# Optimization experiments

Measured on AMD Instinct MI355X. Metric: run time of the kernel, lower is better.

## Reference

```python
import jax, jax.numpy as jnp
import numpy as np

B, S, DM, H = 16, 4096, 512, 4
HD = DM // H  # head_dim = 128
EPS = 1e-5


def setup_inputs() -> dict:
    key = jax.random.key(0)
    ks = jax.random.split(key, 9)
    sc = 1.0 / np.sqrt(DM)
    inp = {
        "x": jax.random.normal(ks[0], (B, S, DM), dtype=jnp.float32),
        "Wq_w": jax.random.normal(ks[1], (DM, DM), dtype=jnp.float32) * sc,
        "Wq_b": jnp.zeros((DM,), dtype=jnp.float32),
        "Wk_w": jax.random.normal(ks[2], (DM, DM), dtype=jnp.float32) * sc,
        "Wk_b": jnp.zeros((DM,), dtype=jnp.float32),
        "Wv_w": jax.random.normal(ks[3], (DM, DM), dtype=jnp.float32) * sc,
        "Wv_b": jnp.zeros((DM,), dtype=jnp.float32),
        "Wo_w": jax.random.normal(ks[4], (DM, DM), dtype=jnp.float32) * sc,
        "Wo_b": jnp.zeros((DM,), dtype=jnp.float32),
        "ln_g": jnp.ones((DM,), dtype=jnp.float32),
        "ln_b": jnp.zeros((DM,), dtype=jnp.float32),
    }
    return inp


def _forward(x, Wq_w, Wq_b, Wk_w, Wk_b, Wv_w, Wv_b, Wo_w, Wo_b, ln_g, ln_b):
    b, s, _ = x.shape
    # Linear projections, viewed as [B,S,H,HD] exactly as the torch code does
    Q = (x @ Wq_w.T + Wq_b).reshape(b, s, H, HD)
    K = (x @ Wk_w.T + Wk_b).reshape(b, s, H, HD)
    V = (x @ Wv_w.T + Wv_b).reshape(b, s, H, HD)
    # NOTE: source never permutes heads to dim 1, so attention is over the
    # HEAD axis per token: scores [B,S,H,H]
    scores = jnp.einsum("bshd,bstd->bsht", Q, K) / np.sqrt(HD).astype(np.float32)
    attn = jax.nn.softmax(scores, axis=-1)  # dropout is identity in eval
    out = jnp.einsum("bsht,bstd->bshd", attn, V).reshape(b, s, DM)
    out = out @ Wo_w.T + Wo_b
    y = out + x  # input_dim == output_dim -> residual branch taken
    mu = jnp.mean(y, axis=-1, keepdims=True)
    var = jnp.mean((y - mu) ** 2, axis=-1, keepdims=True)
    return (y - mu) * jax.lax.rsqrt(var + EPS) * ln_g + ln_b


def reference(x, Wq_w, Wq_b, Wk_w, Wk_b, Wv_w, Wv_b, Wo_w, Wo_b, ln_g, ln_b):
    return _forward(x, Wq_w, Wq_b, Wk_w, Wk_b, Wv_w, Wv_b, Wo_w, Wo_b, ln_g, ln_b)
```

## Files before the change

kernel.cpp:

```cpp
#include <hip/hip_runtime.h>
#include <stdint.h>

#define NTOK 65536
#define DMODEL 512
#define QKVN 1536
#define LN_EPS 1e-5f

typedef __attribute__((ext_vector_type(8))) short short8;
typedef __attribute__((ext_vector_type(8))) unsigned short ushort8;
typedef __attribute__((ext_vector_type(4))) float float4_t;

static __device__ __forceinline__ float bf2f(unsigned short u) {
    union { unsigned int i; float f; } c; c.i = ((unsigned int)u) << 16; return c.f;
}
static __device__ __forceinline__ unsigned short f2bf(float f) {
    union { float f; unsigned int i; } c; c.f = f;
    unsigned int x = c.i;
    return (unsigned short)((x + 0x7fffu + ((x >> 16) & 1u)) >> 16);
}
static __device__ __forceinline__ void gload_lds16(const void* g, void* l) {
    __builtin_amdgcn_global_load_lds((const __attribute__((address_space(1))) void*)g,
                                     (__attribute__((address_space(3))) void*)l, 16, 0, 0);
}

#define BAR() __builtin_amdgcn_s_barrier()
#define WAITL0() asm volatile("s_waitcnt lgkmcnt(0)" ::: "memory")
#define WVM(n) asm volatile("s_waitcnt vmcnt(" #n ")" ::: "memory")
#define MFMA(a, b, c) __builtin_amdgcn_mfma_f32_16x16x32_bf16((a), (b), (c), 0, 0, 0)

__global__ __launch_bounds__(256) void cast_x_kernel(const float* __restrict__ x,
                                                     unsigned short* __restrict__ xb, int n8) {
    int stride = gridDim.x * blockDim.x;
    for (int i = blockIdx.x * blockDim.x + threadIdx.x; i < n8; i += stride) {
        const float4_t* p = (const float4_t*)(x + (size_t)i * 8);
        float4_t a = p[0], b = p[1];
        ushort8 v;
        v[0] = f2bf(a[0]); v[1] = f2bf(a[1]); v[2] = f2bf(a[2]); v[3] = f2bf(a[3]);
        v[4] = f2bf(b[0]); v[5] = f2bf(b[1]); v[6] = f2bf(b[2]); v[7] = f2bf(b[3]);
        *(ushort8*)(xb + (size_t)i * 8) = v;
    }
}

__global__ __launch_bounds__(256) void prep_w_kernel(
    const float* __restrict__ wq, const float* __restrict__ wk, const float* __restrict__ wv,
    const float* __restrict__ wo,
    const float* __restrict__ bq, const float* __restrict__ bk, const float* __restrict__ bv,
    unsigned short* __restrict__ wqkv, unsigned short* __restrict__ wob,
    float* __restrict__ bias_qkv) {
    const int WN = DMODEL * DMODEL;
    int tid = blockIdx.x * blockDim.x + threadIdx.x;
    int stride = gridDim.x * blockDim.x;
    for (int j = tid; j < 3 * WN; j += stride) {
        int seg = j / WN, idx = j - seg * WN;
        const float* src = (seg == 0) ? wq : (seg == 1) ? wk : wv;
        wqkv[j] = f2bf(src[idx]);
    }
    for (int j = tid; j < WN; j += stride) wob[j] = f2bf(wo[j]);
    for (int j = tid; j < QKVN; j += stride)
        bias_qkv[j] = (j < 512) ? bq[j] : (j < 1024) ? bk[j - 512] : bv[j - 1024];
}

__global__ __launch_bounds__(512, 2) void gemm1_kernel(
    const unsigned short* __restrict__ A, const unsigned short* __restrict__ Bw,
    const float* __restrict__ bias, unsigned short* __restrict__ Cout) {
    __shared__ unsigned short As[4][256 * 32];
    __shared__ unsigned short Bs[4][256 * 32];

    const int b = blockIdx.x;
    const int L = (b & 7) * 192 + (b >> 3);
    const int bm = L / 6;
    const int bn = L - bm * 6;

    const int t = threadIdx.x;
    const int lane = t & 63;
    const int w = t >> 6;
    const int wm = w >> 2, wn = w & 3;

    const unsigned short* Ab = A + (size_t)bm * 256 * 512;
    const unsigned short* Bb = Bw + (size_t)bn * 256 * 512;

    const int i0 = t, i1 = 512 + t;
    const int r0 = i0 >> 2, s0 = (i0 & 3) ^ ((r0 >> 1) & 3);
    const int r1 = i1 >> 2, s1 = (i1 & 3) ^ ((r1 >> 1) & 3);

#define STAGE_A1(kt) do { \
        gload_lds16(Ab + r0 * 512 + (kt) * 32 + s0 * 8, &As[(kt) & 3][i0 * 8]); \
        gload_lds16(Ab + r1 * 512 + (kt) * 32 + s1 * 8, &As[(kt) & 3][i1 * 8]); } while (0)
#define STAGE_B1(kt) do { \
        gload_lds16(Bb + r0 * 512 + (kt) * 32 + s0 * 8, &Bs[(kt) & 3][i0 * 8]); \
        gload_lds16(Bb + r1 * 512 + (kt) * 32 + s1 * 8, &Bs[(kt) & 3][i1 * 8]); } while (0)

    int aoff[8], boff[4];
#pragma unroll
    for (int m = 0; m < 8; m++) {
        int row = wm * 128 + m * 16 + (lane & 15);
        aoff[m] = row * 32 + (((lane >> 4) ^ ((row >> 1) & 3)) * 8);
    }
#pragma unroll
    for (int n = 0; n < 4; n++) {
        int row = wn * 64 + n * 16 + (lane & 15);
        boff[n] = row * 32 + (((lane >> 4) ^ ((row >> 1) & 3)) * 8);
    }

    float4_t acc[8][4];
#pragma unroll
    for (int m = 0; m < 8; m++)
#pragma unroll
        for (int n = 0; n < 4; n++) acc[m][n] = (float4_t){0.f, 0.f, 0.f, 0.f};

    STAGE_A1(0); STAGE_B1(0);
    STAGE_A1(1); STAGE_B1(1);
    STAGE_A1(2); STAGE_B1(2);
    WVM(8);
    BAR();

    short8 ar[8], br[4];
#pragma unroll
    for (int kt = 0; kt < 16; ++kt) {
        const int sl = kt & 3;
#pragma unroll
        for (int m = 0; m < 8; m++) ar[m] = *(const short8*)&As[sl][aoff[m]];
        br[0] = *(const short8*)&Bs[sl][boff[0]];
        br[1] = *(const short8*)&Bs[sl][boff[1]];
        if (kt <= 12) STAGE_A1(kt + 3);
        BAR();
        WAITL0();
        __builtin_amdgcn_s_setprio(1);
#pragma unroll
        for (int m = 0; m < 8; m++) {
            acc[m][0] = MFMA(ar[m], br[0], acc[m][0]);
            acc[m][1] = MFMA(ar[m], br[1], acc[m][1]);
        }
        __builtin_amdgcn_s_setprio(0);
        BAR();
        br[2] = *(const short8*)&Bs[sl][boff[2]];
        br[3] = *(const short8*)&Bs[sl][boff[3]];
        if (kt <= 12) STAGE_B1(kt + 3);
        BAR();
        WAITL0();
        __builtin_amdgcn_s_setprio(1);
#pragma unroll
        for (int m = 0; m < 8; m++) {
            acc[m][2] = MFMA(ar[m], br[2], acc[m][2]);
            acc[m][3] = MFMA(ar[m], br[3], acc[m][3]);
        }
        __builtin_amdgcn_s_setprio(0);
        if (kt <= 12) { WVM(8); }
        else if (kt == 13) { WVM(4); }
        else if (kt == 14) { WVM(0); }
        BAR();
    }

    const int orow0 = bm * 256 + wm * 128;
    const int ocol0 = bn * 256 + wn * 64;
#pragma unroll
    for (int m = 0; m < 8; m++) {
#pragma unroll
        for (int n = 0; n < 4; n++) {
            int col = ocol0 + n * 16 + (lane & 15);
            float bv = bias[col];
#pragma unroll
            for (int j = 0; j < 4; j++) {
                int row = orow0 + m * 16 + (lane >> 4) * 4 + j;
                Cout[(size_t)row * QKVN + col] = f2bf(acc[m][n][j] + bv);
            }
        }
    }
#undef STAGE_A1
#undef STAGE_B1
}

__global__ __launch_bounds__(256) void attn_kernel(const unsigned short* __restrict__ qkv,
                                                   unsigned short* __restrict__ out) {
    const int tok = blockIdx.x * 4 + (threadIdx.x >> 6);
    const int lane = threadIdx.x & 63;
    const unsigned short* base = qkv + (size_t)tok * QKVN;

    float q[4][2], k[4][2], v[4][2];
#pragma unroll
    for (int h = 0; h < 4; h++) {
        unsigned int uq = *(const unsigned int*)(base + h * 128 + 2 * lane);
        unsigned int uk = *(const unsigned int*)(base + 512 + h * 128 + 2 * lane);
        unsigned int uv = *(const unsigned int*)(base + 1024 + h * 128 + 2 * lane);
        q[h][0] = bf2f((unsigned short)(uq & 0xffff)); q[h][1] = bf2f((unsigned short)(uq >> 16));
        k[h][0] = bf2f((unsigned short)(uk & 0xffff)); k[h][1] = bf2f((unsigned short)(uk >> 16));
        v[h][0] = bf2f((unsigned short)(uv & 0xffff)); v[h][1] = bf2f((unsigned short)(uv >> 16));
    }

    float s[4][4];
#pragma unroll
    for (int h = 0; h < 4; h++)
#pragma unroll
        for (int tt = 0; tt < 4; tt++)
            s[h][tt] = q[h][0] * k[tt][0] + q[h][1] * k[tt][1];

#pragma unroll
    for (int mask = 1; mask < 64; mask <<= 1) {
#pragma unroll
        for (int h = 0; h < 4; h++)
#pragma unroll
            for (int tt = 0; tt < 4; tt++)
                s[h][tt] += __shfl_xor(s[h][tt], mask, 64);
    }

    const float scale = 0.08838834764831845f;
    float p[4][4];
#pragma unroll
    for (int h = 0; h < 4; h++) {
        float m0 = fmaxf(fmaxf(s[h][0], s[h][1]), fmaxf(s[h][2], s[h][3])) * scale;
        float sum = 0.f;
#pragma unroll
        for (int tt = 0; tt < 4; tt++) { p[h][tt] = __expf(s[h][tt] * scale - m0); sum += p[h][tt]; }
        float r = __frcp_rn(sum);
#pragma unroll
        for (int tt = 0; tt < 4; tt++) p[h][tt] *= r;
    }

#pragma unroll
    for (int h = 0; h < 4; h++) {
        float o0 = 0.f, o1 = 0.f;
#pragma unroll
        for (int tt = 0; tt < 4; tt++) { o0 += p[h][tt] * v[tt][0]; o1 += p[h][tt] * v[tt][1]; }
        unsigned int packed = (unsigned int)f2bf(o0) | ((unsigned int)f2bf(o1) << 16);
        *(unsigned int*)(out + (size_t)tok * 512 + h * 128 + 2 * lane) = packed;
    }
}

__global__ __launch_bounds__(512, 2) void gemm2_ln_kernel(
    const unsigned short* __restrict__ AO, const unsigned short* __restrict__ Wob,
    const float* __restrict__ bo, const float* __restrict__ xres,
    const float* __restrict__ lng, const float* __restrict__ lnb,
    float* __restrict__ Y) {
    __shared__ __align__(16) unsigned short smem[3 * 4096 + 3 * 16384];
    unsigned short* As = smem;
    unsigned short* Bs = smem + 3 * 4096;
    float* red = (float*)smem;

    const int bm = blockIdx.x;
    const int t = threadIdx.x;
    const int lane = t & 63;
    const int wn = t >> 6;

    const unsigned short* Ab = AO + (size_t)bm * 128 * 512;

    const int ar_ = t >> 2, as_ = (t & 3) ^ ((ar_ >> 1) & 3);
#define STAGE_A2(kt) gload_lds16(Ab + ar_ * 512 + (kt) * 32 + as_ * 8, &As[((kt) % 3) * 4096 + t * 8])
#define STAGE_B2(kt, l) do { \
        int idx_ = (l) * 512 + t; int row_ = idx_ >> 2; int ss_ = (idx_ & 3) ^ ((row_ >> 1) & 3); \
        gload_lds16(Wob + row_ * 512 + (kt) * 32 + ss_ * 8, &Bs[((kt) % 3) * 16384 + idx_ * 8]); } while (0)

    int aoff[8], boff[4];
#pragma unroll
    for (int m = 0; m < 8; m++) {
        int row = m * 16 + (lane & 15);
        aoff[m] = row * 32 + (((lane >> 4) ^ ((row >> 1) & 3)) * 8);
    }
#pragma unroll
    for (int n = 0; n < 4; n++) {
        int row = wn * 64 + n * 16 + (lane & 15);
        boff[n] = row * 32 + (((lane >> 4) ^ ((row >> 1) & 3)) * 8);
    }

    float4_t acc[8][4];
#pragma unroll
    for (int m = 0; m < 8; m++)
#pragma unroll
        for (int n = 0; n < 4; n++) acc[m][n] = (float4_t){0.f, 0.f, 0.f, 0.f};

    STAGE_A2(0); STAGE_B2(0, 0); STAGE_B2(0, 1); STAGE_B2(0, 2); STAGE_B2(0, 3);
    STAGE_A2(1); STAGE_B2(1, 0); STAGE_B2(1, 1); STAGE_B2(1, 2); STAGE_B2(1, 3);
    WVM(5);
    BAR();

    short8 ar[8], br[4];
#pragma unroll
    for (int kt = 0; kt < 16; ++kt) {
        const int sl = kt % 3;
#pragma unroll
        for (int m = 0; m < 8; m++) ar[m] = *(const short8*)&As[sl * 4096 + aoff[m]];
        br[0] = *(const short8*)&Bs[sl * 16384 + boff[0]];
        br[1] = *(const short8*)&Bs[sl * 16384 + boff[1]];
        if (kt <= 13) { STAGE_A2(kt + 2); STAGE_B2(kt + 2, 0); STAGE_B2(kt + 2, 1); }
        BAR();
        WAITL0();
        __builtin_amdgcn_s_setprio(1);
#pragma unroll
        for (int m = 0; m < 8; m++) {
            acc[m][0] = MFMA(ar[m], br[0], acc[m][0]);
            acc[m][1] = MFMA(ar[m], br[1], acc[m][1]);
        }
        __builtin_amdgcn_s_setprio(0);
        BAR();
        br[2] = *(const short8*)&Bs[sl * 16384 + boff[2]];
        br[3] = *(const short8*)&Bs[sl * 16384 + boff[3]];
        if (kt <= 13) { STAGE_B2(kt + 2, 2); STAGE_B2(kt + 2, 3); }
        BAR();
        WAITL0();
        __builtin_amdgcn_s_setprio(1);
#pragma unroll
        for (int m = 0; m < 8; m++) {
            acc[m][2] = MFMA(ar[m], br[2], acc[m][2]);
            acc[m][3] = MFMA(ar[m], br[3], acc[m][3]);
        }
        __builtin_amdgcn_s_setprio(0);
        if (kt <= 13) { WVM(5); }
        else if (kt == 14) { WVM(0); }
        BAR();
    }

    __syncthreads();

    float bias4[4], gc4[4], bc4[4];
#pragma unroll
    for (int n = 0; n < 4; n++) {
        int c = wn * 64 + n * 16 + (lane & 15);
        bias4[n] = bo[c]; gc4[n] = lng[c]; bc4[n] = lnb[c];
    }
#pragma unroll
    for (int m = 0; m < 8; m++) {
#pragma unroll
        for (int j = 0; j < 4; j++) {
            int grow = bm * 128 + m * 16 + (lane >> 4) * 4 + j;
            const float* xr = xres + (size_t)grow * 512;
#pragma unroll
            for (int n = 0; n < 4; n++) {
                int c = wn * 64 + n * 16 + (lane & 15);
                acc[m][n][j] += bias4[n] + xr[c];
            }
        }
    }
#pragma unroll
    for (int m = 0; m < 8; m++) {
#pragma unroll
        for (int j = 0; j < 4; j++) {
            float s = 0.f, s2 = 0.f;
#pragma unroll
            for (int n = 0; n < 4; n++) { float v = acc[m][n][j]; s += v; s2 += v * v; }
#pragma unroll
            for (int mask = 1; mask < 16; mask <<= 1) {
                s += __shfl_xor(s, mask, 64);
                s2 += __shfl_xor(s2, mask, 64);
            }
            if ((lane & 15) == 0) {
                int rl = m * 16 + (lane >> 4) * 4 + j;
                red[(wn * 128 + rl) * 2 + 0] = s;
                red[(wn * 128 + rl) * 2 + 1] = s2;
            }
        }
    }
    __syncthreads();
#pragma unroll
    for (int m = 0; m < 8; m++) {
#pragma unroll
        for (int j = 0; j < 4; j++) {
            int rl = m * 16 + (lane >> 4) * 4 + j;
            float s = 0.f, s2 = 0.f;
#pragma unroll
            for (int i = 0; i < 8; i++) {
                s += red[(i * 128 + rl) * 2 + 0];
                s2 += red[(i * 128 + rl) * 2 + 1];
            }
            float mu = s * (1.f / 512.f);
            float var = s2 * (1.f / 512.f) - mu * mu;
            float inv = rsqrtf(var + LN_EPS);
            int grow = bm * 128 + rl;
            float* yp = Y + (size_t)grow * 512;
#pragma unroll
            for (int n = 0; n < 4; n++) {
                int c = wn * 64 + n * 16 + (lane & 15);
                yp[c] = (acc[m][n][j] - mu) * inv * gc4[n] + bc4[n];
            }
        }
    }
#undef STAGE_A2
#undef STAGE_B2
}

extern "C" void kernel_launch(void* const* d_in, const int* in_sizes, int n_in,
                              void* d_out, int out_size, void* d_ws, size_t ws_size,
                              hipStream_t stream) {
    const float* x   = (const float*)d_in[0];
    const float* wq  = (const float*)d_in[1];
    const float* bq  = (const float*)d_in[2];
    const float* wk  = (const float*)d_in[3];
    const float* bk  = (const float*)d_in[4];
    const float* wv  = (const float*)d_in[5];
    const float* bv  = (const float*)d_in[6];
    const float* wo  = (const float*)d_in[7];
    const float* bo  = (const float*)d_in[8];
    const float* lng = (const float*)d_in[9];
    const float* lnb = (const float*)d_in[10];

    char* ws = (char*)d_ws;
    unsigned short* Xb   = (unsigned short*)(ws);
    unsigned short* Wqkv = (unsigned short*)(ws + 67108864);
    unsigned short* Wob  = (unsigned short*)(ws + 68681728);
    float*          Bqkv = (float*)        (ws + 69206016);
    unsigned short* QKV  = (unsigned short*)(ws + 69212160);
    unsigned short* AO   = (unsigned short*)(ws + 270538752);
    float* Y = (float*)d_out;

    cast_x_kernel<<<2048, 256, 0, stream>>>(x, Xb, NTOK * 512 / 8);
    prep_w_kernel<<<1024, 256, 0, stream>>>(wq, wk, wv, wo, bq, bk, bv, Wqkv, Wob, Bqkv);

    gemm1_kernel<<<(NTOK / 256) * (QKVN / 256), 512, 0, stream>>>(Xb, Wqkv, Bqkv, QKV);

    attn_kernel<<<NTOK / 4, 256, 0, stream>>>(QKV, AO);

    gemm2_ln_kernel<<<NTOK / 128, 512, 0, stream>>>(AO, Wob, bo, x, lng, lnb, Y);
}
```

Measured before the change: 388.6 us.

## Rewrite output GEMM+LayerNorm to load pre-packed MFMA fragments directly from global

Pre-packs the output projection weight into MFMA fragment order during weight prep. The output GEMM then drops LDS staging and barriers, with each wave loading A and B fragments straight from global memory. It uses smaller 32-row tiles with 256 threads, so there are more blocks and higher occupancy. This removes LDS traffic and synchronisation overhead, but every block rereads the full weight matrix from L2 and issues uncoalesced row loads.

New measurement: 410.3 us. 1.06x slower.

```diff
diff --git a/kernel.cpp b/kernel.cpp
--- a/kernel.cpp
+++ b/kernel.cpp
@@ -45,7 +45,7 @@
     const float* __restrict__ wq, const float* __restrict__ wk, const float* __restrict__ wv,
     const float* __restrict__ wo,
     const float* __restrict__ bq, const float* __restrict__ bk, const float* __restrict__ bv,
-    unsigned short* __restrict__ wqkv, unsigned short* __restrict__ wob,
+    unsigned short* __restrict__ wqkv, unsigned short* __restrict__ wpack,
     float* __restrict__ bias_qkv) {
     const int WN = DMODEL * DMODEL;
     int tid = blockIdx.x * blockDim.x + threadIdx.x;
@@ -55,7 +55,12 @@
         const float* src = (seg == 0) ? wq : (seg == 1) ? wk : wv;
         wqkv[j] = f2bf(src[idx]);
     }
-    for (int j = tid; j < WN; j += stride) wob[j] = f2bf(wo[j]);
+    for (int j = tid; j < WN; j += stride) {
+        int e = j & 7, l = (j >> 3) & 63, nf = (j >> 9) & 31, kt = j >> 14;
+        int row = nf * 16 + (l & 15);
+        int k = kt * 32 + ((l >> 4) << 3) + e;
+        wpack[j] = f2bf(wo[row * 512 + k]);
+    }
     for (int j = tid; j < QKVN; j += stride)
         bias_qkv[j] = (j < 512) ? bq[j] : (j < 1024) ? bk[j - 512] : bv[j - 1024];
 }
@@ -226,116 +231,70 @@
     }
 }
 
-__global__ __launch_bounds__(512, 2) void gemm2_ln_kernel(
-    const unsigned short* __restrict__ AO, const unsigned short* __restrict__ Wob,
+__global__ __launch_bounds__(256) void gemm2_ln_kernel(
+    const unsigned short* __restrict__ AO, const unsigned short* __restrict__ Wpack,
     const float* __restrict__ bo, const float* __restrict__ xres,
     const float* __restrict__ lng, const float* __restrict__ lnb,
     float* __restrict__ Y) {
-    __shared__ __align__(16) unsigned short smem[3 * 4096 + 3 * 16384];
-    unsigned short* As = smem;
-    unsigned short* Bs = smem + 3 * 4096;
-    float* red = (float*)smem;
-
-    const int bm = blockIdx.x;
+    __shared__ float red[4][32][2];
+
+    const int blk = blockIdx.x;
     const int t = threadIdx.x;
     const int lane = t & 63;
     const int wn = t >> 6;
-
-    const unsigned short* Ab = AO + (size_t)bm * 128 * 512;
-
-    const int ar_ = t >> 2, as_ = (t & 3) ^ ((ar_ >> 1) & 3);
-#define STAGE_A2(kt) gload_lds16(Ab + ar_ * 512 + (kt) * 32 + as_ * 8, &As[((kt) % 3) * 4096 + t * 8])
-#define STAGE_B2(kt, l) do { \
-        int idx_ = (l) * 512 + t; int row_ = idx_ >> 2; int ss_ = (idx_ & 3) ^ ((row_ >> 1) & 3); \
-        gload_lds16(Wob + row_ * 512 + (kt) * 32 + ss_ * 8, &Bs[((kt) % 3) * 16384 + idx_ * 8]); } while (0)
-
-    int aoff[8], boff[4];
-#pragma unroll
-    for (int m = 0; m < 8; m++) {
-        int row = m * 16 + (lane & 15);
-        aoff[m] = row * 32 + (((lane >> 4) ^ ((row >> 1) & 3)) * 8);
-    }
-#pragma unroll
-    for (int n = 0; n < 4; n++) {
-        int row = wn * 64 + n * 16 + (lane & 15);
-        boff[n] = row * 32 + (((lane >> 4) ^ ((row >> 1) & 3)) * 8);
-    }
-
-    float4_t acc[8][4];
-#pragma unroll
-    for (int m = 0; m < 8; m++)
-#pragma unroll
-        for (int n = 0; n < 4; n++) acc[m][n] = (float4_t){0.f, 0.f, 0.f, 0.f};
-
-    STAGE_A2(0); STAGE_B2(0, 0); STAGE_B2(0, 1); STAGE_B2(0, 2); STAGE_B2(0, 3);
-    STAGE_A2(1); STAGE_B2(1, 0); STAGE_B2(1, 1); STAGE_B2(1, 2); STAGE_B2(1, 3);
-    WVM(5);
-    BAR();
-
-    short8 ar[8], br[4];
-#pragma unroll
+    const int R0 = blk * 32;
+
+    const unsigned short* Abase =
+        AO + ((size_t)R0 + (lane & 15)) * 512 + (lane >> 4) * 8;
+    const unsigned short* Bbase = Wpack + ((size_t)(wn * 8) * 64 + lane) * 8;
+
+    float4_t acc[2][8];
+#pragma unroll
+    for (int m = 0; m < 2; m++)
+#pragma unroll
+        for (int n = 0; n < 8; n++) acc[m][n] = (float4_t){0.f, 0.f, 0.f, 0.f};
+
+#pragma unroll 2
     for (int kt = 0; kt < 16; ++kt) {
-        const int sl = kt % 3;
-#pragma unroll
-        for (int m = 0; m < 8; m++) ar[m] = *(const short8*)&As[sl * 4096 + aoff[m]];
-        br[0] = *(const short8*)&Bs[sl * 16384 + boff[0]];
-        br[1] = *(const short8*)&Bs[sl * 16384 + boff[1]];
-        if (kt <= 13) { STAGE_A2(kt + 2); STAGE_B2(kt + 2, 0); STAGE_B2(kt + 2, 1); }
-        BAR();
-        WAITL0();
-        __builtin_amdgcn_s_setprio(1);
-#pragma unroll
-        for (int m = 0; m < 8; m++) {
-            acc[m][0] = MFMA(ar[m], br[0], acc[m][0]);
-            acc[m][1] = MFMA(ar[m], br[1], acc[m][1]);
-        }
-        __builtin_amdgcn_s_setprio(0);
-        BAR();
-        br[2] = *(const short8*)&Bs[sl * 16384 + boff[2]];
-        br[3] = *(const short8*)&Bs[sl * 16384 + boff[3]];
-        if (kt <= 13) { STAGE_B2(kt + 2, 2); STAGE_B2(kt + 2, 3); }
-        BAR();
-        WAITL0();
-        __builtin_amdgcn_s_setprio(1);
-#pragma unroll
-        for (int m = 0; m < 8; m++) {
-            acc[m][2] = MFMA(ar[m], br[2], acc[m][2]);
-            acc[m][3] = MFMA(ar[m], br[3], acc[m][3]);
-        }
-        __builtin_amdgcn_s_setprio(0);
-        if (kt <= 13) { WVM(5); }
-        else if (kt == 14) { WVM(0); }
-        BAR();
-    }
-
-    __syncthreads();
-
-    float bias4[4], gc4[4], bc4[4];
-#pragma unroll
-    for (int n = 0; n < 4; n++) {
-        int c = wn * 64 + n * 16 + (lane & 15);
-        bias4[n] = bo[c]; gc4[n] = lng[c]; bc4[n] = lnb[c];
-    }
-#pragma unroll
-    for (int m = 0; m < 8; m++) {
+        short8 a0 = *(const short8*)(Abase + kt * 32);
+        short8 a1 = *(const short8*)(Abase + 16 * 512 + kt * 32);
+        short8 bfr[8];
+#pragma unroll
+        for (int n = 0; n < 8; n++)
+            bfr[n] = *(const short8*)(Bbase + (size_t)kt * 16384 + n * 512);
+#pragma unroll
+        for (int n = 0; n < 8; n++) {
+            acc[0][n] = MFMA(a0, bfr[n], acc[0][n]);
+            acc[1][n] = MFMA(a1, bfr[n], acc[1][n]);
+        }
+    }
+
+    float bias8[8], gc8[8], bc8[8];
+#pragma unroll
+    for (int n = 0; n < 8; n++) {
+        int c = wn * 128 + n * 16 + (lane & 15);
+        bias8[n] = bo[c]; gc8[n] = lng[c]; bc8[n] = lnb[c];
+    }
+#pragma unroll
+    for (int m = 0; m < 2; m++) {
 #pragma unroll
         for (int j = 0; j < 4; j++) {
-            int grow = bm * 128 + m * 16 + (lane >> 4) * 4 + j;
+            int grow = R0 + m * 16 + (lane >> 4) * 4 + j;
             const float* xr = xres + (size_t)grow * 512;
 #pragma unroll
-            for (int n = 0; n < 4; n++) {
-                int c = wn * 64 + n * 16 + (lane & 15);
-                acc[m][n][j] += bias4[n] + xr[c];
-            }
-        }
-    }
-#pragma unroll
-    for (int m = 0; m < 8; m++) {
+            for (int n = 0; n < 8; n++) {
+                int c = wn * 128 + n * 16 + (lane & 15);
+                acc[m][n][j] += bias8[n] + xr[c];
+            }
+        }
+    }
+#pragma unroll
+    for (int m = 0; m < 2; m++) {
 #pragma unroll
         for (int j = 0; j < 4; j++) {
             float s = 0.f, s2 = 0.f;
 #pragma unroll
-            for (int n = 0; n < 4; n++) { float v = acc[m][n][j]; s += v; s2 += v * v; }
+            for (int n = 0; n < 8; n++) { float v = acc[m][n][j]; s += v; s2 += v * v; }
 #pragma unroll
             for (int mask = 1; mask < 16; mask <<= 1) {
                 s += __shfl_xor(s, mask, 64);
@@ -343,37 +302,31 @@
             }
             if ((lane & 15) == 0) {
                 int rl = m * 16 + (lane >> 4) * 4 + j;
-                red[(wn * 128 + rl) * 2 + 0] = s;
-                red[(wn * 128 + rl) * 2 + 1] = s2;
+                red[wn][rl][0] = s;
+                red[wn][rl][1] = s2;
             }
         }
     }
     __syncthreads();
 #pragma unroll
-    for (int m = 0; m < 8; m++) {
+    for (int m = 0; m < 2; m++) {
 #pragma unroll
         for (int j = 0; j < 4; j++) {
             int rl = m * 16 + (lane >> 4) * 4 + j;
-            float s = 0.f, s2 = 0.f;
-#pragma unroll
-            for (int i = 0; i < 8; i++) {
-                s += red[(i * 128 + rl) * 2 + 0];
-                s2 += red[(i * 128 + rl) * 2 + 1];
-            }
+            float s = red[0][rl][0] + red[1][rl][0] + red[2][rl][0] + red[3][rl][0];
+            float s2 = red[0][rl][1] + red[1][rl][1] + red[2][rl][1] + red[3][rl][1];
             float mu = s * (1.f / 512.f);
             float var = s2 * (1.f / 512.f) - mu * mu;
             float inv = rsqrtf(var + LN_EPS);
-            int grow = bm * 128 + rl;
+            int grow = R0 + rl;
             float* yp = Y + (size_t)grow * 512;
 #pragma unroll
-            for (int n = 0; n < 4; n++) {
-                int c = wn * 64 + n * 16 + (lane & 15);
-                yp[c] = (acc[m][n][j] - mu) * inv * gc4[n] + bc4[n];
-            }
-        }
-    }
-#undef STAGE_A2
-#undef STAGE_B2
+            for (int n = 0; n < 8; n++) {
+                int c = wn * 128 + n * 16 + (lane & 15);
+                yp[c] = (acc[m][n][j] - mu) * inv * gc8[n] + bc8[n];
+            }
+        }
+    }
 }
 
 extern "C" void kernel_launch(void* const* d_in, const int* in_sizes, int n_in,
@@ -392,20 +345,20 @@
     const float* lnb = (const float*)d_in[10];
 
     char* ws = (char*)d_ws;
-    unsigned short* Xb   = (unsigned short*)(ws);
-    unsigned short* Wqkv = (unsigned short*)(ws + 67108864);
-    unsigned short* Wob  = (unsigned short*)(ws + 68681728);
-    float*          Bqkv = (float*)        (ws + 69206016);
-    unsigned short* QKV  = (unsigned short*)(ws + 69212160);
-    unsigned short* AO   = (unsigned short*)(ws + 270538752);
+    unsigned short* Xb    = (unsigned short*)(ws);
+    unsigned short* Wqkv  = (unsigned short*)(ws + 67108864);
+    unsigned short* Wpack = (unsigned short*)(ws + 68681728);
+    float*          Bqkv  = (float*)        (ws + 69206016);
+    unsigned short* QKV   = (unsigned short*)(ws + 69212160);
+    unsigned short* AO    = (unsigned short*)(ws + 270538752);
     float* Y = (float*)d_out;
 
     cast_x_kernel<<<2048, 256, 0, stream>>>(x, Xb, NTOK * 512 / 8);
-    prep_w_kernel<<<1024, 256, 0, stream>>>(wq, wk, wv, wo, bq, bk, bv, Wqkv, Wob, Bqkv);
+    prep_w_kernel<<<1024, 256, 0, stream>>>(wq, wk, wv, wo, bq, bk, bv, Wqkv, Wpack, Bqkv);
 
     gemm1_kernel<<<(NTOK / 256) * (QKVN / 256), 512, 0, stream>>>(Xb, Wqkv, Bqkv, QKV);
 
     attn_kernel<<<NTOK / 4, 256, 0, stream>>>(QKV, AO);
 
-    gemm2_ln_kernel<<<NTOK / 128, 512, 0, stream>>>(AO, Wob, bo, x, lng, lnb, Y);
-}
+    gemm2_ln_kernel<<<NTOK / 32, 256, 0, stream>>>(AO, Wpack, bo, x, lng, lnb, Y);
+}
```
